# Kernel optimization log

Measured on AMD Instinct MI355X. Metric: run time of the kernel, lower is better.

Reference implementation:

```python
import jax, jax.numpy as jnp
import numpy as np

C = 512
H_HEADS = 8
CTX_D = 768
GEO_D = 512
FFN_D = 4 * C
EPS = 1e-5


def _layernorm(x, g, b):
    mu = jnp.mean(x, axis=-1, keepdims=True)
    var = jnp.mean((x - mu) ** 2, axis=-1, keepdims=True)
    return (x - mu) * jax.lax.rsqrt(var + EPS) * g + b


def _cross_attn(x, ctx, Wq, Wk, Wv, Wo, bo, h):
    # x: (B, N, C), ctx: (B, S, Dctx)
    b, n, _ = x.shape
    s = ctx.shape[1]
    inner = Wq.shape[1]
    d = inner // h
    q = (x @ Wq).reshape(b, n, h, d)
    k = (ctx @ Wk).reshape(b, s, h, d)
    v = (ctx @ Wv).reshape(b, s, h, d)
    sim = jnp.einsum('bihd,bjhd->bhij', q, k) * (d ** -0.5)
    attn = jax.nn.softmax(sim, axis=-1)
    out = jnp.einsum('bhij,bjhd->bihd', attn, v).reshape(b, n, inner)
    return out @ Wo + bo


def setup_inputs() -> dict:
    key = jax.random.key(0)
    ks = jax.random.split(key, 24)
    std = lambda fan_in: 1.0 / np.sqrt(fan_in)
    inp = {
        'x': jax.random.normal(ks[0], (4, C, 64, 64), jnp.float32),
        'context': jax.random.normal(ks[1], (4, 77, CTX_D), jnp.float32),
        'geometry_tokens': jax.random.normal(ks[2], (4, 256, GEO_D), jnp.float32),
        # layernorm params (norm1..norm4)
        'g1': jnp.ones((C,)), 'b1': jnp.zeros((C,)),
        'g2': jnp.ones((C,)), 'b2': jnp.zeros((C,)),
        'g3': jnp.ones((C,)), 'b3': jnp.zeros((C,)),
        'g4': jnp.ones((C,)), 'b4': jnp.zeros((C,)),
        # cross-attention (context) weights
        'cWq': jax.random.normal(ks[3], (C, C)) * std(C),
        'cWk': jax.random.normal(ks[4], (CTX_D, C)) * std(CTX_D),
        'cWv': jax.random.normal(ks[5], (CTX_D, C)) * std(CTX_D),
        'cWo': jax.random.normal(ks[6], (C, C)) * std(C),
        'cbo': jnp.zeros((C,)),
        # geometry-attention weights
        'gWq': jax.random.normal(ks[7], (C, C)) * std(C),
        'gWk': jax.random.normal(ks[8], (GEO_D, C)) * std(GEO_D),
        'gWv': jax.random.normal(ks[9], (GEO_D, C)) * std(GEO_D),
        'gWo': jax.random.normal(ks[10], (C, C)) * std(C),
        'gbo': jnp.zeros((C,)),
        # FFN weights
        'W1': jax.random.normal(ks[11], (C, FFN_D)) * std(C),
        'bf1': jnp.zeros((FFN_D,)),
        'W2': jax.random.normal(ks[12], (FFN_D, C)) * std(FFN_D),
        'bf2': jnp.zeros((C,)),
    }
    return inp


def reference(x, context, geometry_tokens,
              g1, b1, g2, b2, g3, b3, g4, b4,
              cWq, cWk, cWv, cWo, cbo,
              gWq, gWk, gWv, gWo, gbo,
              W1, bf1, W2, bf2):
    b, c, h, w = x.shape
    t = x.reshape(b, c, h * w).transpose(0, 2, 1)  # (B, N, C)
    # self_attn is called with context=None -> identity, so this is t + norm1(t)
    t = t + _layernorm(t, g1, b1)
    t = t + _cross_attn(_layernorm(t, g2, b2), context, cWq, cWk, cWv, cWo, cbo, H_HEADS)
    t = t + _cross_attn(_layernorm(t, g3, b3), geometry_tokens, gWq, gWk, gWv, gWo, gbo, H_HEADS)
    hdn = jax.nn.gelu(_layernorm(t, g4, b4) @ W1 + bf1, approximate=False)
    t = t + hdn @ W2 + bf2
    return t.transpose(0, 2, 1).reshape(b, c, h, w)
```

## Files before the change

### kernel.cpp

```cpp
#include <hip/hip_runtime.h>
#include <hip/hip_bf16.h>

using bf16 = __hip_bfloat16;
typedef __attribute__((ext_vector_type(8))) short short8;
typedef __attribute__((ext_vector_type(4))) short short4v;
typedef __attribute__((ext_vector_type(4))) float floatx4;

#define DEVFN __device__ __forceinline__

DEVFN float bf2f(bf16 v) { return __bfloat162float(v); }
DEVFN bf16 f2bf(float v) { return __float2bfloat16(v); }
DEVFN float us2f(unsigned short u) {
    union { unsigned int i; float f; } c; c.i = ((unsigned int)u) << 16; return c.f;
}
DEVFN unsigned short f2bfbits(float v) {
    union { bf16 h; unsigned short u; } c; c.h = f2bf(v); return c.u;
}
DEVFN float loadF(const void* p, size_t i, int isf) {
    return isf ? ((const float*)p)[i] : us2f(((const unsigned short*)p)[i]);
}
DEVFN void gl_lds16(const bf16* g, short* l) {
    __builtin_amdgcn_global_load_lds(
        (const __attribute__((address_space(1))) unsigned int*)g,
        (__attribute__((address_space(3))) unsigned int*)l, 16, 0, 0);
}
DEVFN float fast_gelu(float v) {
    float u = v * (0.7978845608028654f + 0.0356774081f * v * v);
    float e = __expf(2.f * u);
    float th = 1.f - 2.f / (e + 1.f);
    return 0.5f * v * (1.f + th);
}

__global__ __launch_bounds__(256) void detect_kernel(const void* x, int* flag)
{
    __shared__ int any;
    if (threadIdx.x == 0) any = 0;
    __syncthreads();
    const unsigned short* p = (const unsigned short*)x;
    int hit = 0;
    for (int i = threadIdx.x; i < 8192; i += 256) {
        if ((p[i] & 0x7F80u) == 0x7F80u) hit = 1;
    }
    if (hit) any = 1;
    __syncthreads();
    if (threadIdx.x == 0) flag[0] = any;
}

__global__ __launch_bounds__(256) void convert_kernel(
    const void* __restrict__ src, bf16* __restrict__ dst, const int* __restrict__ flag, int n)
{
    int isf = *flag;
    int i = blockIdx.x * 256 + threadIdx.x;
    if (i < n) dst[i] = f2bf(loadF(src, i, isf));
}

struct SegTab {
    const void* src[12];
    int off[12];
    int cnt[12];
};
__global__ __launch_bounds__(256) void param_convert_kernel(
    SegTab tab, bf16* __restrict__ dst, const int* __restrict__ flag)
{
    int isf = *flag;
    int s = blockIdx.x;
    const void* src = tab.src[s];
    int off = tab.off[s], cnt = tab.cnt[s];
    for (int i = threadIdx.x; i < cnt; i += 256)
        dst[off + i] = f2bf(loadF(src, i, isf));
}

__global__ __launch_bounds__(256) void ln_in_kernel(
    const void* __restrict__ x, float* __restrict__ t,
    const bf16* __restrict__ g, const bf16* __restrict__ bta,
    const int* __restrict__ flag, int NN)
{
    __shared__ float tile[16][516];
    int isf = *flag;
    int b = blockIdx.y;
    int n0 = blockIdx.x * 16;
    int tid = threadIdx.x;
    int nx = tid & 15, cy = tid >> 4;
#pragma unroll
    for (int p = 0; p < 32; p++) {
        int c = p * 16 + cy;
        tile[nx][c] = loadF(x, ((size_t)b * 512 + c) * NN + n0 + nx, isf);
    }
    __syncthreads();
    int w = tid >> 6, lane = tid & 63;
    for (int rr = 0; rr < 4; rr++) {
        int r = w * 4 + rr;
        float4 v0 = *(const float4*)&tile[r][lane * 8];
        float4 v1 = *(const float4*)&tile[r][lane * 8 + 4];
        float vals[8] = {v0.x, v0.y, v0.z, v0.w, v1.x, v1.y, v1.z, v1.w};
        float s = 0.f;
#pragma unroll
        for (int i = 0; i < 8; i++) s += vals[i];
#pragma unroll
        for (int off = 32; off; off >>= 1) s += __shfl_xor(s, off, 64);
        float mu = s * (1.f / 512.f);
        float sq = 0.f;
#pragma unroll
        for (int i = 0; i < 8; i++) { float d = vals[i] - mu; sq += d * d; }
#pragma unroll
        for (int off = 32; off; off >>= 1) sq += __shfl_xor(sq, off, 64);
        float rs = rsqrtf(sq * (1.f / 512.f) + 1e-5f);
        float out[8];
#pragma unroll
        for (int i = 0; i < 8; i++) {
            int c = lane * 8 + i;
            out[i] = vals[i] + (vals[i] - mu) * rs * bf2f(g[c]) + bf2f(bta[c]);
        }
        float* tp = t + ((size_t)b * NN + n0 + r) * 512 + lane * 8;
        *(float4*)tp = make_float4(out[0], out[1], out[2], out[3]);
        *(float4*)(tp + 4) = make_float4(out[4], out[5], out[6], out[7]);
    }
}

__global__ __launch_bounds__(256) void transpose_out_kernel(
    const float* __restrict__ t, void* __restrict__ o, const int* __restrict__ flag,
    int C, int NN)
{
    __shared__ float tile[32][33];
    int isf = *flag;
    int b = blockIdx.z;
    int n0 = blockIdx.x * 32, c0 = blockIdx.y * 32;
    int tx = threadIdx.x, ty = threadIdx.y;
#pragma unroll
    for (int i = 0; i < 4; i++)
        tile[ty + i * 8][tx] = t[((size_t)b * NN + n0 + ty + i * 8) * C + c0 + tx];
    __syncthreads();
#pragma unroll
    for (int i = 0; i < 4; i++) {
        size_t oi = ((size_t)b * C + c0 + ty + i * 8) * NN + n0 + tx;
        float val = tile[tx][ty + i * 8];
        if (isf) ((float*)o)[oi] = val;
        else ((bf16*)o)[oi] = f2bf(val);
    }
}

__global__ __launch_bounds__(256) void transpose_w_kernel(
    const void* __restrict__ Wm, bf16* __restrict__ WT, const int* __restrict__ flag,
    int K, int Nc)
{
    __shared__ float tile[32][33];
    int isf = *flag;
    int n0 = blockIdx.x * 32, k0 = blockIdx.y * 32;
    int tx = threadIdx.x, ty = threadIdx.y;
#pragma unroll
    for (int i = 0; i < 4; i++)
        tile[ty + i * 8][tx] = loadF(Wm, (size_t)(k0 + ty + i * 8) * Nc + n0 + tx, isf);
    __syncthreads();
#pragma unroll
    for (int i = 0; i < 4; i++)
        WT[(size_t)(n0 + ty + i * 8) * K + k0 + tx] = f2bf(tile[tx][ty + i * 8]);
}

__global__ __launch_bounds__(256) void ln_kernel(
    const float* __restrict__ t, const bf16* __restrict__ g, const bf16* __restrict__ bta,
    bf16* __restrict__ outp, int Mrows)
{
    int w = threadIdx.x >> 6, lane = threadIdx.x & 63;
    int row = blockIdx.x * 4 + w;
    if (row >= Mrows) return;
    const float* xr = t + (size_t)row * 512;
    float4 v0 = *(const float4*)(xr + lane * 8);
    float4 v1 = *(const float4*)(xr + lane * 8 + 4);
    float vals[8] = {v0.x, v0.y, v0.z, v0.w, v1.x, v1.y, v1.z, v1.w};
    float s = 0.f;
#pragma unroll
    for (int i = 0; i < 8; i++) s += vals[i];
#pragma unroll
    for (int off = 32; off; off >>= 1) s += __shfl_xor(s, off, 64);
    float mu = s * (1.f / 512.f);
    float sq = 0.f;
#pragma unroll
    for (int i = 0; i < 8; i++) { float d = vals[i] - mu; sq += d * d; }
#pragma unroll
    for (int off = 32; off; off >>= 1) sq += __shfl_xor(sq, off, 64);
    float rs = rsqrtf(sq * (1.f / 512.f) + 1e-5f);
#pragma unroll
    for (int i = 0; i < 8; i++) {
        int c = lane * 8 + i;
        float y = (vals[i] - mu) * rs * bf2f(g[c]) + bf2f(bta[c]);
        outp[(size_t)row * 512 + c] = f2bf(y);
    }
}

template <int MODE>
__global__ __launch_bounds__(256) void gemm64(
    const bf16* __restrict__ A, const bf16* __restrict__ WT,
    const bf16* __restrict__ bias, void* __restrict__ outp,
    int M, int K, int Nc)
{
    __shared__ short As[64 * 32];
    __shared__ short Bs[64 * 32];
    const int tid = threadIdx.x;
    const int m0 = blockIdx.y * 64;
    const int n0 = blockIdx.x * 64;
    const int w = tid >> 6;
    const int lane = tid & 63;
    const int lm = lane & 15;
    const int lq = lane >> 4;

    floatx4 acc[4];
#pragma unroll
    for (int nb = 0; nb < 4; nb++) acc[nb] = (floatx4){0.f, 0.f, 0.f, 0.f};

    const int srow = tid >> 2;
    const int scol = (tid & 3) << 3;
    const int agrow = m0 + srow;
    const bool aok = agrow < M;
    const bf16* Aptr = A + (size_t)agrow * K + scol;
    const bf16* Bptr = WT + (size_t)(n0 + srow) * K + scol;

    for (int k0 = 0; k0 < K; k0 += 32) {
        __syncthreads();
        int4 av = make_int4(0, 0, 0, 0);
        if (aok) av = *(const int4*)(Aptr + k0);
        *(int4*)(&As[srow * 32 + scol]) = av;
        *(int4*)(&Bs[srow * 32 + scol]) = *(const int4*)(Bptr + k0);
        __syncthreads();
        short8 a = *(const short8*)(&As[(w * 16 + lm) * 32 + lq * 8]);
#pragma unroll
        for (int nb = 0; nb < 4; nb++) {
            short8 b = *(const short8*)(&Bs[(nb * 16 + lm) * 32 + lq * 8]);
            acc[nb] = __builtin_amdgcn_mfma_f32_16x16x32_bf16(a, b, acc[nb], 0, 0, 0);
        }
    }

#pragma unroll
    for (int nb = 0; nb < 4; nb++) {
        int col = n0 + nb * 16 + lm;
        float bv = bias ? bf2f(bias[col]) : 0.f;
#pragma unroll
        for (int r = 0; r < 4; r++) {
            int row = m0 + w * 16 + lq * 4 + r;
            if (row < M) {
                float v = acc[nb][r] + bv;
                if (MODE == 1) v = fast_gelu(v);
                if (MODE == 2) {
                    ((float*)outp)[(size_t)row * Nc + col] += v;
                } else {
                    ((bf16*)outp)[(size_t)row * Nc + col] = f2bf(v);
                }
            }
        }
    }
}

template <int MODE>
__global__ __launch_bounds__(256) void gemm128(
    const bf16* __restrict__ A, const bf16* __restrict__ WT,
    const bf16* __restrict__ bias, void* __restrict__ outp,
    int K, int Nc)
{
    __shared__ short As[128 * 32];
    __shared__ short Bs[128 * 32];
    const int tid = threadIdx.x;
    const int m0 = blockIdx.y * 128;
    const int n0 = blockIdx.x * 128;
    const int w = tid >> 6, lane = tid & 63;
    const int lm = lane & 15, lq = lane >> 4;
    const int wy = w >> 1, wx = w & 1;

    floatx4 acc[4][4];
#pragma unroll
    for (int cb = 0; cb < 4; cb++)
#pragma unroll
        for (int rb = 0; rb < 4; rb++) acc[cb][rb] = (floatx4){0.f, 0.f, 0.f, 0.f};

    const int c0 = w * 2, c1 = w * 2 + 1;
    const int lr = lane >> 2;
    const int lk = (((lane & 3) ^ (lr & 3)) << 3);
    const bf16* gA0 = A + (size_t)(m0 + c0 * 16 + lr) * K + lk;
    const bf16* gA1 = A + (size_t)(m0 + c1 * 16 + lr) * K + lk;
    const bf16* gB0 = WT + (size_t)(n0 + c0 * 16 + lr) * K + lk;
    const bf16* gB1 = WT + (size_t)(n0 + c1 * 16 + lr) * K + lk;
    short* lA0 = &As[c0 * 512];
    short* lA1 = &As[c1 * 512];
    short* lB0 = &Bs[c0 * 512];
    short* lB1 = &Bs[c1 * 512];

    const int fsw = ((lq ^ (lm & 3)) * 8);
    for (int k0 = 0; k0 < K; k0 += 32) {
        gl_lds16(gA0 + k0, lA0);
        gl_lds16(gA1 + k0, lA1);
        gl_lds16(gB0 + k0, lB0);
        gl_lds16(gB1 + k0, lB1);
        __syncthreads();
        short8 wf[4], xf[4];
#pragma unroll
        for (int cb = 0; cb < 4; cb++)
            wf[cb] = *(const short8*)(&Bs[(wx * 64 + cb * 16 + lm) * 32 + fsw]);
#pragma unroll
        for (int rb = 0; rb < 4; rb++)
            xf[rb] = *(const short8*)(&As[(wy * 64 + rb * 16 + lm) * 32 + fsw]);
#pragma unroll
        for (int cb = 0; cb < 4; cb++)
#pragma unroll
            for (int rb = 0; rb < 4; rb++)
                acc[cb][rb] = __builtin_amdgcn_mfma_f32_16x16x32_bf16(wf[cb], xf[rb], acc[cb][rb], 0, 0, 0);
        __syncthreads();
    }

    float4 bias4[4];
#pragma unroll
    for (int cb = 0; cb < 4; cb++) {
        if (bias) {
            const bf16* bp = bias + n0 + wx * 64 + cb * 16 + lq * 4;
            bias4[cb] = make_float4(bf2f(bp[0]), bf2f(bp[1]), bf2f(bp[2]), bf2f(bp[3]));
        } else {
            bias4[cb] = make_float4(0.f, 0.f, 0.f, 0.f);
        }
    }

    if (MODE == 2) {
        float* po = (float*)outp;
#pragma unroll
        for (int rb = 0; rb < 4; rb++) {
            size_t m = m0 + wy * 64 + rb * 16 + lm;
#pragma unroll
            for (int cb = 0; cb < 4; cb++) {
                float* p = po + m * Nc + n0 + wx * 64 + cb * 16 + lq * 4;
                float4 f = *(float4*)p;
                f.x += acc[cb][rb][0] + bias4[cb].x;
                f.y += acc[cb][rb][1] + bias4[cb].y;
                f.z += acc[cb][rb][2] + bias4[cb].z;
                f.w += acc[cb][rb][3] + bias4[cb].w;
                *(float4*)p = f;
            }
        }
    } else {
        unsigned short* stg = (unsigned short*)&As[w * 1024];
        unsigned short* op = (unsigned short*)outp;
#pragma unroll
        for (int rb = 0; rb < 4; rb++) {
#pragma unroll
            for (int cb = 0; cb < 4; cb++) {
                short4v pk;
#pragma unroll
                for (int r = 0; r < 4; r++) {
                    float vv = acc[cb][rb][r] + ((const float*)&bias4[cb])[r];
                    if (MODE == 1) vv = fast_gelu(vv);
                    pk[r] = (short)f2bfbits(vv);
                }
                int chunk = (cb * 2 + (lq >> 1)) ^ (lm & 7);
                *(short4v*)(&stg[lm * 64 + chunk * 8 + (lq & 1) * 4]) = pk;
            }
#pragma unroll
            for (int p = 0; p < 2; p++) {
                int row = p * 8 + (lane >> 3);
                int chunk = lane & 7;
                short8 ov = *(const short8*)(&stg[row * 64 + ((chunk ^ (row & 7)) * 8)]);
                size_t m = m0 + wy * 64 + rb * 16 + row;
                *(short8*)(op + m * Nc + n0 + wx * 64 + chunk * 8) = ov;
            }
        }
    }
}

template <int SPAD, int SVALID>
__global__ __launch_bounds__(256) void attn_mfma_kernel(
    const bf16* __restrict__ q, const bf16* __restrict__ k, const bf16* __restrict__ v,
    bf16* __restrict__ o, int N)
{
    constexpr int MB = SPAD / 16;
    constexpr int KS = SPAD / 32;
    __shared__ unsigned short lds[SPAD * 64 + 64 * SPAD];
    unsigned short* Ks = lds;
    unsigned short* Vt = lds + SPAD * 64;
    unsigned short* Pw = lds;

    const int tid = threadIdx.x;
    const int b = blockIdx.x >> 3;
    const int h = blockIdx.x & 7;
    const int n0 = blockIdx.y * 64;
    const int w = tid >> 6, lane = tid & 63;
    const int lm = lane & 15, lq = lane >> 4;

    const unsigned short* kp = (const unsigned short*)k;
    const unsigned short* vp = (const unsigned short*)v;
    for (int idx = tid * 8; idx < SPAD * 64; idx += 2048) {
        int s = idx >> 6, d0 = idx & 63;
        short8 kv = {0, 0, 0, 0, 0, 0, 0, 0};
        short8 vv = {0, 0, 0, 0, 0, 0, 0, 0};
        if (s < SVALID) {
            size_t gb = ((size_t)(b * SVALID + s)) * 512 + h * 64 + d0;
            kv = *(const short8*)(kp + gb);
            vv = *(const short8*)(vp + gb);
        }
        int kc = (d0 >> 3) ^ (s & 7);
        *(short8*)(&Ks[s * 64 + kc * 8]) = kv;
        const unsigned short* vvp = (const unsigned short*)&vv;
#pragma unroll
        for (int i = 0; i < 8; i++) {
            int d = d0 + i;
            int sc = (s >> 3) ^ (d & 7);
            Vt[d * SPAD + sc * 8 + (s & 7)] = vvp[i];
        }
    }

    const int q0 = n0 + w * 16;
    const unsigned short* qp = (const unsigned short*)q;
    size_t qbase = ((size_t)(b * N + q0 + lm)) * 512 + h * 64 + lq * 8;
    short8 qf0 = *(const short8*)(qp + qbase);
    short8 qf1 = *(const short8*)(qp + qbase + 32);
    __syncthreads();

    floatx4 sacc[MB];
#pragma unroll
    for (int mb = 0; mb < MB; mb++) sacc[mb] = (floatx4){0.f, 0.f, 0.f, 0.f};
#pragma unroll
    for (int mb = 0; mb < MB; mb++) {
        int srow = mb * 16 + lm;
        short8 a0 = *(const short8*)(&Ks[srow * 64 + ((lq ^ (lm & 7)) * 8)]);
        short8 a1 = *(const short8*)(&Ks[srow * 64 + (((4 + lq) ^ (lm & 7)) * 8)]);
        sacc[mb] = __builtin_amdgcn_mfma_f32_16x16x32_bf16(a0, qf0, sacc[mb], 0, 0, 0);
        sacc[mb] = __builtin_amdgcn_mfma_f32_16x16x32_bf16(a1, qf1, sacc[mb], 0, 0, 0);
    }

    float mx = -1e30f;
#pragma unroll
    for (int mb = 0; mb < MB; mb++)
#pragma unroll
        for (int r = 0; r < 4; r++) {
            int s = mb * 16 + lq * 4 + r;
            if (s < SVALID) mx = fmaxf(mx, sacc[mb][r]);
        }
    mx = fmaxf(mx, __shfl_xor(mx, 16, 64));
    mx = fmaxf(mx, __shfl_xor(mx, 32, 64));
    mx *= 0.125f;
    float sum = 0.f;
#pragma unroll
    for (int mb = 0; mb < MB; mb++)
#pragma unroll
        for (int r = 0; r < 4; r++) {
            int s = mb * 16 + lq * 4 + r;
            float e = (s < SVALID) ? __expf(sacc[mb][r] * 0.125f - mx) : 0.f;
            sacc[mb][r] = e;
            sum += e;
        }
    sum += __shfl_xor(sum, 16, 64);
    sum += __shfl_xor(sum, 32, 64);
    float inv = 1.f / sum;

    __syncthreads();

    unsigned short* Pme = Pw + w * 16 * SPAD;
#pragma unroll
    for (int mb = 0; mb < MB; mb++) {
        short4v pk;
        pk[0] = (short)f2bfbits(sacc[mb][0] * inv);
        pk[1] = (short)f2bfbits(sacc[mb][1] * inv);
        pk[2] = (short)f2bfbits(sacc[mb][2] * inv);
        pk[3] = (short)f2bfbits(sacc[mb][3] * inv);
        int chunk = (mb * 2 + (lq >> 1)) ^ (lm & 7);
        *(short4v*)(&Pme[lm * SPAD + chunk * 8 + (lq & 1) * 4]) = pk;
    }

    floatx4 oacc[4];
#pragma unroll
    for (int mb2 = 0; mb2 < 4; mb2++) oacc[mb2] = (floatx4){0.f, 0.f, 0.f, 0.f};
    for (int ks = 0; ks < KS; ks++) {
        int sch = ((ks * 4 + lq) ^ (lm & 7)) * 8;
        short8 bfrag = *(const short8*)(&Pme[lm * SPAD + sch]);
#pragma unroll
        for (int mb2 = 0; mb2 < 4; mb2++) {
            int d = mb2 * 16 + lm;
            short8 afrag = *(const short8*)(&Vt[d * SPAD + sch]);
            oacc[mb2] = __builtin_amdgcn_mfma_f32_16x16x32_bf16(afrag, bfrag, oacc[mb2], 0, 0, 0);
        }
    }

#pragma unroll
    for (int mb2 = 0; mb2 < 4; mb2++) {
        short4v ok;
        ok[0] = (short)f2bfbits(oacc[mb2][0]);
        ok[1] = (short)f2bfbits(oacc[mb2][1]);
        ok[2] = (short)f2bfbits(oacc[mb2][2]);
        ok[3] = (short)f2bfbits(oacc[mb2][3]);
        int chunk = (mb2 * 2 + (lq >> 1)) ^ (lm & 7);
        *(short4v*)(&Pme[lm * 64 + chunk * 8 + (lq & 1) * 4]) = ok;
    }
    unsigned short* op = (unsigned short*)o;
#pragma unroll
    for (int p = 0; p < 2; p++) {
        int row = p * 8 + (lane >> 3);
        int chunk = lane & 7;
        short8 ov = *(const short8*)(&Pme[row * 64 + ((chunk ^ (row & 7)) * 8)]);
        *(short8*)(op + ((size_t)(b * N + n0 + w * 16 + row)) * 512 + h * 64 + chunk * 8) = ov;
    }
}

extern "C" void kernel_launch(void* const* d_in, const int* in_sizes, int n_in,
                              void* d_out, int out_size, void* d_ws, size_t ws_size,
                              hipStream_t stream)
{
    const void* x   = d_in[0];
    const void* ctx = d_in[1];
    const void* geo = d_in[2];
    const void* g1 = d_in[3];  const void* b1 = d_in[4];
    const void* g2 = d_in[5];  const void* b2 = d_in[6];
    const void* g3 = d_in[7];  const void* b3 = d_in[8];
    const void* g4 = d_in[9];  const void* b4 = d_in[10];
    const void* cWq = d_in[11]; const void* cWk = d_in[12];
    const void* cWv = d_in[13]; const void* cWo = d_in[14];
    const void* cbo = d_in[15];
    const void* gWq = d_in[16]; const void* gWk = d_in[17];
    const void* gWv = d_in[18]; const void* gWo = d_in[19];
    const void* gbo = d_in[20];
    const void* W1 = d_in[21];  const void* bf1 = d_in[22];
    const void* W2 = d_in[23];  const void* bf2 = d_in[24];

    const int B = 4, C = 512, NN = 4096;
    const int M = B * NN;

    char* ws = (char*)d_ws;
    size_t off = 0;
    auto alloc = [&](size_t bytes) -> void* {
        void* p = ws + off; off += (bytes + 255) & ~(size_t)255; return p;
    };
    int*   flag = (int*)alloc(256);
    float* t  = (float*)alloc((size_t)M * C * 4);
    bf16* u   = (bf16*)alloc((size_t)M * C * 2);
    bf16* qb  = (bf16*)alloc((size_t)M * C * 2);
    bf16* kb  = (bf16*)alloc((size_t)B * 256 * C * 2);
    bf16* vb  = (bf16*)alloc((size_t)B * 256 * C * 2);
    bf16* ctxb = (bf16*)alloc((size_t)B * 77 * 768 * 2);
    bf16* geob = (bf16*)alloc((size_t)B * 256 * 512 * 2);
    bf16* cWqT = (bf16*)alloc((size_t)512 * 512 * 2);
    bf16* cWkT = (bf16*)alloc((size_t)512 * 768 * 2);
    bf16* cWvT = (bf16*)alloc((size_t)512 * 768 * 2);
    bf16* cWoT = (bf16*)alloc((size_t)512 * 512 * 2);
    bf16* gWqT = (bf16*)alloc((size_t)512 * 512 * 2);
    bf16* gWkT = (bf16*)alloc((size_t)512 * 512 * 2);
    bf16* gWvT = (bf16*)alloc((size_t)512 * 512 * 2);
    bf16* gWoT = (bf16*)alloc((size_t)512 * 512 * 2);
    bf16* W1T  = (bf16*)alloc((size_t)2048 * 512 * 2);
    bf16* W2T  = (bf16*)alloc((size_t)512 * 2048 * 2);
    bf16* prm  = (bf16*)alloc((size_t)7680 * 2);
    bf16* ob = u;

    int chunk;
    bf16* hb;
    size_t rem = (ws_size > off) ? (ws_size - off) : 0;
    if (rem >= (size_t)16384 * 2048 * 2) { chunk = 16384; hb = (bf16*)alloc((size_t)16384 * 2048 * 2); }
    else if (rem >= (size_t)8192 * 2048 * 2) { chunk = 8192; hb = (bf16*)alloc((size_t)8192 * 2048 * 2); }
    else { chunk = 4096; hb = qb; }
    (void)in_sizes; (void)n_in; (void)out_size;

    bf16 *pg1 = prm, *pb1 = prm + 512, *pg2 = prm + 1024, *pb2 = prm + 1536;
    bf16 *pg3 = prm + 2048, *pb3 = prm + 2560, *pg4 = prm + 3072, *pb4 = prm + 3584;
    bf16 *pcbo = prm + 4096, *pgbo = prm + 4608, *pbf1 = prm + 5120, *pbf2 = prm + 7168;

    dim3 tb(32, 8);

    detect_kernel<<<1, 256, 0, stream>>>(x, flag);
    SegTab tab;
    const void* srcs[12] = {g1, b1, g2, b2, g3, b3, g4, b4, cbo, gbo, bf1, bf2};
    int offs[12] = {0, 512, 1024, 1536, 2048, 2560, 3072, 3584, 4096, 4608, 5120, 7168};
    int cnts[12] = {512, 512, 512, 512, 512, 512, 512, 512, 512, 512, 2048, 512};
    for (int i = 0; i < 12; i++) { tab.src[i] = srcs[i]; tab.off[i] = offs[i]; tab.cnt[i] = cnts[i]; }
    param_convert_kernel<<<12, 256, 0, stream>>>(tab, prm, flag);
    convert_kernel<<<(B * 77 * 768 + 255) / 256, 256, 0, stream>>>(ctx, ctxb, flag, B * 77 * 768);
    convert_kernel<<<(B * 256 * 512 + 255) / 256, 256, 0, stream>>>(geo, geob, flag, B * 256 * 512);

    ln_in_kernel<<<dim3(NN / 16, B), 256, 0, stream>>>(x, t, pg1, pb1, flag, NN);

    transpose_w_kernel<<<dim3(512 / 32, 512 / 32), tb, 0, stream>>>(cWq, cWqT, flag, 512, 512);
    transpose_w_kernel<<<dim3(512 / 32, 768 / 32), tb, 0, stream>>>(cWk, cWkT, flag, 768, 512);
    transpose_w_kernel<<<dim3(512 / 32, 768 / 32), tb, 0, stream>>>(cWv, cWvT, flag, 768, 512);
    transpose_w_kernel<<<dim3(512 / 32, 512 / 32), tb, 0, stream>>>(cWo, cWoT, flag, 512, 512);
    transpose_w_kernel<<<dim3(512 / 32, 512 / 32), tb, 0, stream>>>(gWq, gWqT, flag, 512, 512);
    transpose_w_kernel<<<dim3(512 / 32, 512 / 32), tb, 0, stream>>>(gWk, gWkT, flag, 512, 512);
    transpose_w_kernel<<<dim3(512 / 32, 512 / 32), tb, 0, stream>>>(gWv, gWvT, flag, 512, 512);
    transpose_w_kernel<<<dim3(512 / 32, 512 / 32), tb, 0, stream>>>(gWo, gWoT, flag, 512, 512);
    transpose_w_kernel<<<dim3(2048 / 32, 512 / 32), tb, 0, stream>>>(W1, W1T, flag, 512, 2048);
    transpose_w_kernel<<<dim3(512 / 32, 2048 / 32), tb, 0, stream>>>(W2, W2T, flag, 2048, 512);

    ln_kernel<<<M / 4, 256, 0, stream>>>(t, pg2, pb2, u, M);
    gemm128<0><<<dim3(4, M / 128), 256, 0, stream>>>(u, cWqT, nullptr, qb, 512, 512);
    gemm64<0><<<dim3(8, (308 + 63) / 64), 256, 0, stream>>>(ctxb, cWkT, nullptr, kb, 308, 768, 512);
    gemm64<0><<<dim3(8, (308 + 63) / 64), 256, 0, stream>>>(ctxb, cWvT, nullptr, vb, 308, 768, 512);
    attn_mfma_kernel<128, 77><<<dim3(B * 8, NN / 64), 256, 0, stream>>>(qb, kb, vb, ob, NN);
    gemm128<2><<<dim3(4, M / 128), 256, 0, stream>>>(ob, cWoT, pcbo, t, 512, 512);

    ln_kernel<<<M / 4, 256, 0, stream>>>(t, pg3, pb3, u, M);
    gemm128<0><<<dim3(4, M / 128), 256, 0, stream>>>(u, gWqT, nullptr, qb, 512, 512);
    gemm64<0><<<dim3(8, 1024 / 64), 256, 0, stream>>>(geob, gWkT, nullptr, kb, 1024, 512, 512);
    gemm64<0><<<dim3(8, 1024 / 64), 256, 0, stream>>>(geob, gWvT, nullptr, vb, 1024, 512, 512);
    attn_mfma_kernel<256, 256><<<dim3(B * 8, NN / 64), 256, 0, stream>>>(qb, kb, vb, ob, NN);
    gemm128<2><<<dim3(4, M / 128), 256, 0, stream>>>(ob, gWoT, pgbo, t, 512, 512);

    ln_kernel<<<M / 4, 256, 0, stream>>>(t, pg4, pb4, u, M);
    for (int mc = 0; mc < M / chunk; mc++) {
        bf16* uc = u + (size_t)mc * chunk * 512;
        float* tc = t + (size_t)mc * chunk * 512;
        gemm128<1><<<dim3(2048 / 128, chunk / 128), 256, 0, stream>>>(uc, W1T, pbf1, hb, 512, 2048);
        gemm128<2><<<dim3(512 / 128, chunk / 128), 256, 0, stream>>>(hb, W2T, pbf2, tc, 2048, 512);
    }

    transpose_out_kernel<<<dim3(NN / 32, C / 32, B), tb, 0, stream>>>(t, d_out, flag, C, NN);
}
```

Measured before the change: 548.8 us.

## Triple-buffer LDS tiles in gemm128 with async prefetch two stages ahead

Replaces the single LDS buffer in the 128x128 GEMM with a three-stage ring, issuing global-to-LDS loads two k-tiles ahead. Each iteration uses one barrier with a partial vmcnt wait instead of two full syncs. It also raises wave priority around the MFMA block. The goal is to hide global load latency behind matrix math, at the cost of triple the LDS footprint and possibly lower occupancy.

```diff
diff --git a/kernel.cpp b/kernel.cpp
--- a/kernel.cpp
+++ b/kernel.cpp
@@ -255,8 +255,8 @@
     const bf16* __restrict__ bias, void* __restrict__ outp,
     int K, int Nc)
 {
-    __shared__ short As[128 * 32];
-    __shared__ short Bs[128 * 32];
+    __shared__ short As[3 * 128 * 32];
+    __shared__ short Bs[3 * 128 * 32];
     const int tid = threadIdx.x;
     const int m0 = blockIdx.y * 128;
     const int n0 = blockIdx.x * 128;
@@ -277,32 +277,52 @@
     const bf16* gA1 = A + (size_t)(m0 + c1 * 16 + lr) * K + lk;
     const bf16* gB0 = WT + (size_t)(n0 + c0 * 16 + lr) * K + lk;
     const bf16* gB1 = WT + (size_t)(n0 + c1 * 16 + lr) * K + lk;
-    short* lA0 = &As[c0 * 512];
-    short* lA1 = &As[c1 * 512];
-    short* lB0 = &Bs[c0 * 512];
-    short* lB1 = &Bs[c1 * 512];
+
+    auto STAGE = [&](int d, int koff) {
+        short* la = As + d * 4096;
+        short* lb = Bs + d * 4096;
+        gl_lds16(gA0 + koff, la + c0 * 512);
+        gl_lds16(gA1 + koff, la + c1 * 512);
+        gl_lds16(gB0 + koff, lb + c0 * 512);
+        gl_lds16(gB1 + koff, lb + c1 * 512);
+    };
+
+    const int nt = K >> 5;
+    STAGE(0, 0);
+    STAGE(1, 32);
+    asm volatile("s_waitcnt vmcnt(4)\n\ts_barrier" ::: "memory");
 
     const int fsw = ((lq ^ (lm & 3)) * 8);
-    for (int k0 = 0; k0 < K; k0 += 32) {
-        gl_lds16(gA0 + k0, lA0);
-        gl_lds16(gA1 + k0, lA1);
-        gl_lds16(gB0 + k0, lB0);
-        gl_lds16(gB1 + k0, lB1);
-        __syncthreads();
+    int cur = 0, stg = 2;
+    for (int t = 0; t < nt; ++t) {
+        if (t + 2 < nt) STAGE(stg, (t + 2) << 5);
+        const short* cA = As + cur * 4096;
+        const short* cB = Bs + cur * 4096;
         short8 wf[4], xf[4];
 #pragma unroll
         for (int cb = 0; cb < 4; cb++)
-            wf[cb] = *(const short8*)(&Bs[(wx * 64 + cb * 16 + lm) * 32 + fsw]);
+            wf[cb] = *(const short8*)(&cB[(wx * 64 + cb * 16 + lm) * 32 + fsw]);
 #pragma unroll
         for (int rb = 0; rb < 4; rb++)
-            xf[rb] = *(const short8*)(&As[(wy * 64 + rb * 16 + lm) * 32 + fsw]);
+            xf[rb] = *(const short8*)(&cA[(wy * 64 + rb * 16 + lm) * 32 + fsw]);
+        __builtin_amdgcn_s_setprio(1);
 #pragma unroll
         for (int cb = 0; cb < 4; cb++)
 #pragma unroll
             for (int rb = 0; rb < 4; rb++)
                 acc[cb][rb] = __builtin_amdgcn_mfma_f32_16x16x32_bf16(wf[cb], xf[rb], acc[cb][rb], 0, 0, 0);
-        __syncthreads();
-    }
+        __builtin_amdgcn_s_setprio(0);
+        if (t + 1 < nt) {
+            if (t + 2 < nt) {
+                asm volatile("s_waitcnt vmcnt(4) lgkmcnt(0)\n\ts_barrier" ::: "memory");
+            } else {
+                asm volatile("s_waitcnt vmcnt(0) lgkmcnt(0)\n\ts_barrier" ::: "memory");
+            }
+        }
+        cur = (cur == 2) ? 0 : cur + 1;
+        stg = (stg == 2) ? 0 : stg + 1;
+    }
+    __syncthreads();
 
     float4 bias4[4];
 #pragma unroll
@@ -332,7 +352,7 @@
             }
         }
     } else {
-        unsigned short* stg = (unsigned short*)&As[w * 1024];
+        unsigned short* stgb = (unsigned short*)&As[w * 1024];
         unsigned short* op = (unsigned short*)outp;
 #pragma unroll
         for (int rb = 0; rb < 4; rb++) {
@@ -346,13 +366,13 @@
                     pk[r] = (short)f2bfbits(vv);
                 }
                 int chunk = (cb * 2 + (lq >> 1)) ^ (lm & 7);
-                *(short4v*)(&stg[lm * 64 + chunk * 8 + (lq & 1) * 4]) = pk;
+                *(short4v*)(&stgb[lm * 64 + chunk * 8 + (lq & 1) * 4]) = pk;
             }
 #pragma unroll
             for (int p = 0; p < 2; p++) {
                 int row = p * 8 + (lane >> 3);
                 int chunk = lane & 7;
-                short8 ov = *(const short8*)(&stg[row * 64 + ((chunk ^ (row & 7)) * 8)]);
+                short8 ov = *(const short8*)(&stgb[row * 64 + ((chunk ^ (row & 7)) * 8)]);
                 size_t m = m0 + wy * 64 + rb * 16 + row;
                 *(short8*)(op + m * Nc + n0 + wx * 64 + chunk * 8) = ov;
             }
```

Measured after the change: 537.0 us. 2.1% less time.
